# Kernel optimization log

Hardware: AMD Instinct MI355X
Metric: run time of the kernel (lower is better)

The kernel has to match this reference:

```python
import jax, jax.numpy as jnp
import numpy as np

CUTOFF = 6.0
NWAVE = 12
NTYPE = 2
DIMS = [36, 256, 128, 64, 32, 1]  # norbit -> hidden -> output


def setup_inputs() -> dict:
    key = jax.random.key(0)
    N, K = 8192, 48
    M = N * K
    ks = jax.random.split(key, 16)
    cart = jax.random.uniform(ks[0], (N, 3), jnp.float32, 0.0, 40.0)
    species = jax.random.randint(ks[1], (N,), 0, NTYPE).astype(jnp.int32)
    center = jnp.repeat(jnp.arange(N, dtype=jnp.int32), K)          # row 0: center atom i
    off = jax.random.randint(ks[2], (M,), 1, N).astype(jnp.int32)
    neigh = jnp.mod(center + off, N)                                 # row 1: neighbor j != i
    neigh_list = jnp.stack([center, neigh], axis=0)
    shifts = jax.random.normal(ks[3], (M, 3), jnp.float32)           # PBC shift vectors
    rs = jnp.tile(jnp.linspace(0.0, CUTOFF, NWAVE, dtype=jnp.float32), (NTYPE, 1))
    inta = -0.5 * jnp.ones((NTYPE, NWAVE), jnp.float32)              # gaussian exponents (negative)
    cparams = jnp.ones((NTYPE, NWAVE), jnp.float32)                  # embedded-atom coefficients
    params = {}
    kidx = 4
    for i in range(4):  # 4 hidden layers, stacked over [3 nets, ntype]
        fi, fo = DIMS[i], DIMS[i + 1]
        params[f'w{i+1}'] = jax.random.normal(ks[kidx], (3, NTYPE, fi, fo), jnp.float32) / np.sqrt(fi)
        params[f'b{i+1}'] = jnp.zeros((3, NTYPE, fo), jnp.float32)
        params[f'a{i+1}'] = jnp.ones((3, NTYPE, fo), jnp.float32)    # Relu_like alpha
        params[f'g{i+1}'] = jnp.ones((3, NTYPE, fo), jnp.float32)    # Relu_like beta
        kidx += 1
    params['wout'] = jax.random.normal(ks[kidx], (3, NTYPE, DIMS[4], 1), jnp.float32) / np.sqrt(DIMS[4])
    params['bout'] = jnp.zeros((3, NTYPE, 1), jnp.float32)
    return dict(cart=cart, shifts=shifts, rs=rs, inta=inta, cparams=cparams,
                **params, species=species, neigh_list=neigh_list)


def density_fn(cart, shifts, rs, inta, cparams, species, neigh_list):
    # EANN GetDensity: radial gaussians * cosine cutoff * angular monomials, scattered to centers.
    N = cart.shape[0]
    i, j = neigh_list[0], neigh_list[1]
    dvec = cart[i] - cart[j] + shifts                                 # [M,3]
    dist = jnp.linalg.norm(dvec, axis=-1)                             # [M]
    fc = jnp.square(0.5 * jnp.cos(dist * (jnp.pi / CUTOFF)) + 0.5)    # cutoff_cosine
    # angular basis: L=0 (1), L=1 (3), L=2 (9) -> 13 components, each premultiplied by fc
    ang = jnp.concatenate([
        fc[:, None],
        fc[:, None] * dvec,
        fc[:, None] * (dvec[:, :, None] * dvec[:, None, :]).reshape(-1, 9),
    ], axis=1)                                                        # [M,13]
    sj = species[j]
    gauss = jnp.exp(inta[sj] * jnp.square(dist[:, None] - rs[sj])) * cparams[sj]  # [M,NWAVE]
    worb = ang[:, :, None] * gauss[:, None, :]                        # [M,13,NWAVE]
    B = jax.ops.segment_sum(worb, i, num_segments=N)                  # [N,13,NWAVE]
    d0 = jnp.square(B[:, 0])                                          # L=0
    d1 = jnp.sum(jnp.square(B[:, 1:4]), axis=1)                       # L=1
    d2 = jnp.sum(jnp.square(B[:, 4:13]), axis=1)                      # L=2
    return jnp.concatenate([d0, d1, d2], axis=1)                      # [N,36]


def net_energy(density, species, layers, wout, bout):
    # per-atom-type MLP with Relu_like activation a*silu(g*x); run all types, select by species
    T = wout.shape[0]
    h = jnp.broadcast_to(density, (T,) + density.shape)               # [T,N,36]
    for (w, b, a, g) in layers:
        h = jnp.einsum('tnf,tfo->tno', h, w) + b[:, None, :]
        h = a[:, None, :] * jax.nn.silu(g[:, None, :] * h)
    out = jnp.einsum('tnf,tfo->tno', h, wout) + bout[:, None, :]      # [T,N,1]
    per_atom = jnp.take_along_axis(out[..., 0].T, species[:, None].astype(jnp.int32), axis=1)[:, 0]
    return jnp.sum(per_atom)


def reference(cart, shifts, rs, inta, cparams,
              w1, b1, a1, g1, w2, b2, a2, g2, w3, b3, a3, g3, w4, b4, a4, g4,
              wout, bout, species, neigh_list):
    def energy(c, n):
        d = density_fn(c, shifts, rs, inta, cparams, species, neigh_list)
        layers = [(w1[n], b1[n], a1[n], g1[n]), (w2[n], b2[n], a2[n], g2[n]),
                  (w3[n], b3[n], a3[n], g3[n]), (w4[n], b4[n], a4[n], g4[n])]
        return net_energy(d, species, layers, wout[n], bout[n])

    jab1 = jax.grad(lambda c: energy(c, 0))(cart)                     # dE0/dcart (create_graph analogue)
    jab2 = jax.grad(lambda c: energy(c, 1))(cart)                     # dE1/dcart
    e2 = energy(cart, 2)
    polar = jnp.einsum('ij,ik->jk', cart, jab1)
    polar = polar + polar.T + jnp.einsum('ij,ik->jk', jab2, jab2)
    polar = polar + e2 * jnp.eye(3, dtype=polar.dtype)
    return polar
```

## Files before the change

kernel.cpp:

```cpp
#include <hip/hip_runtime.h>

#define NWAVE 12
#define NL 13
#define NBW (NL*NWAVE)
#define D0 36
#define D1 256
#define D2 128
#define D3 64
#define D4 32
#define AT 16
#define NMAX 8192
#define NBSC 128
#define PI6 0.52359877559829887307f

#define F4(p) (*(const float4*)(p))
#define F2(p) (*(const float2*)(p))

__device__ __forceinline__ float wave_reduce(float v){
  #pragma unroll
  for(int o=32;o>0;o>>=1) v += __shfl_down(v,o);
  return v;
}

__global__ void perm_kernel(const int* __restrict__ species, int* __restrict__ perm,
                            int* __restrict__ counts, int N){
  __shared__ int sc[256];
  int t = threadIdx.x;
  int per = N/256;
  int c0 = 0;
  for(int k=0;k<per;k++) c0 += (species[t*per+k]==0) ? 1 : 0;
  sc[t]=c0; __syncthreads();
  for(int off=1; off<256; off<<=1){
    int add = (t>=off)? sc[t-off] : 0;
    __syncthreads();
    sc[t] += add;
    __syncthreads();
  }
  int incl = sc[t];
  int excl = incl - c0;
  int total0 = sc[255];
  if(t==0){ counts[0]=total0; counts[1]=N-total0; }
  int base0 = excl;
  int base1 = N + (t*per - excl);
  for(int k=0;k<per;k++){
    int a = t*per+k;
    if(species[a]==0) perm[base0++]=a; else perm[base1++]=a;
  }
}

__global__ void transpose_all_kernel(const float* __restrict__ w1, const float* __restrict__ w2,
                                     const float* __restrict__ w3, const float* __restrict__ w4,
                                     float* __restrict__ t1, float* __restrict__ t2,
                                     float* __restrict__ t3, float* __restrict__ t4){
  const int E1 = 6*D0*D1, E2 = 6*D1*D2, E3 = 6*D2*D3, E4 = 6*D3*D4;
  int idx = blockIdx.x*256 + threadIdx.x;
  if(idx < E1){
    int slab = idx/(D0*D1), r = idx%(D0*D1);
    int f = r/D1, o = r%D1;
    t1[slab*D0*D1 + o*D0 + f] = w1[idx];
  } else if(idx < E1+E2){
    int k = idx-E1; int slab = k/(D1*D2), r = k%(D1*D2);
    int f = r/D2, o = r%D2;
    t2[slab*D1*D2 + o*D1 + f] = w2[k];
  } else if(idx < E1+E2+E3){
    int k = idx-E1-E2; int slab = k/(D2*D3), r = k%(D2*D3);
    int f = r/D3, o = r%D3;
    t3[slab*D2*D3 + o*D2 + f] = w3[k];
  } else if(idx < E1+E2+E3+E4){
    int k = idx-E1-E2-E3; int slab = k/(D3*D4), r = k%(D3*D4);
    int f = r/D4, o = r%D4;
    t4[slab*D3*D4 + o*D3 + f] = w4[k];
  }
}

__global__ void pairs_kernel(const float* __restrict__ cart, const float* __restrict__ shifts,
                             const int* __restrict__ species, const int* __restrict__ neighJ,
                             float4* __restrict__ pairbuf, int M, int N, int K){
  extern __shared__ float4 ca[];
  int t = threadIdx.x;
  for(int a=t; a<N; a+=blockDim.x)
    ca[a] = make_float4(cart[a*3+0], cart[a*3+1], cart[a*3+2], (float)species[a]);
  __syncthreads();
  int stride = gridDim.x*blockDim.x;
  for(int m = blockIdx.x*blockDim.x + t; m < M; m += stride){
    int i = m / K;
    int j = neighJ[m];
    float4 cj = ca[j];
    float4 ci = ca[i];
    float dx = ci.x - cj.x + shifts[m*3+0];
    float dy = ci.y - cj.y + shifts[m*3+1];
    float dz = ci.z - cj.z + shifts[m*3+2];
    float dist = sqrtf(dx*dx+dy*dy+dz*dz);
    float enc = (cj.w != 0.f) ? -dist : dist;
    pairbuf[m] = make_float4(dx, dy, dz, enc);
  }
}

__launch_bounds__(256, 1)
__global__ void density_kernel(const float4* __restrict__ pairbuf,
                               const float* __restrict__ rs, const float* __restrict__ inta,
                               const float* __restrict__ cparams,
                               float* __restrict__ B, int K){
  int wv = threadIdx.x >> 6;
  int t  = threadIdx.x & 63;
  int i  = blockIdx.x*4 + wv;
  __shared__ float sang[4][64][NL];
  __shared__ float sg[4][64][NWAVE];
  if(t < K){
    float4 pb = pairbuf[(size_t)i*K + t];
    float dx = pb.x, dy = pb.y, dz = pb.z;
    int sj = (pb.w < 0.f) ? 1 : 0;
    float dist = fabsf(pb.w);
    float base = 0.5f*cosf(dist*PI6)+0.5f;
    float fc = base*base;
    #pragma unroll
    for(int w=0;w<NWAVE;w++){
      float d = dist - rs[sj*NWAVE+w];
      sg[wv][t][w] = __expf(inta[sj*NWAVE+w]*d*d)*cparams[sj*NWAVE+w];
    }
    sang[wv][t][0]=fc;
    sang[wv][t][1]=fc*dx;  sang[wv][t][2]=fc*dy;  sang[wv][t][3]=fc*dz;
    sang[wv][t][4]=fc*dx*dx; sang[wv][t][5]=fc*dx*dy; sang[wv][t][6]=fc*dx*dz;
    sang[wv][t][7]=fc*dy*dx; sang[wv][t][8]=fc*dy*dy; sang[wv][t][9]=fc*dy*dz;
    sang[wv][t][10]=fc*dz*dx; sang[wv][t][11]=fc*dz*dy; sang[wv][t][12]=fc*dz*dz;
  }
  __syncthreads();
  for(int idx=t; idx<NBW; idx+=64){
    int l = idx/NWAVE, w = idx%NWAVE;
    float s = 0.f;
    for(int k=0;k<K;k++) s += sang[wv][k][l]*sg[wv][k][w];
    B[(size_t)i*NBW+idx] = s;
  }
}

__launch_bounds__(256, 1)
__global__ void mlp_kernel(const float* __restrict__ B,
    const int* __restrict__ perm, const int* __restrict__ counts,
    const float* __restrict__ w1,const float* __restrict__ b1,const float* __restrict__ a1,const float* __restrict__ g1,
    const float* __restrict__ w2,const float* __restrict__ b2,const float* __restrict__ a2,const float* __restrict__ g2,
    const float* __restrict__ w3,const float* __restrict__ b3,const float* __restrict__ a3,const float* __restrict__ g3,
    const float* __restrict__ w4,const float* __restrict__ b4,const float* __restrict__ a4,const float* __restrict__ g4,
    const float* __restrict__ wout,const float* __restrict__ bout,
    const float* __restrict__ wt1,const float* __restrict__ wt2,const float* __restrict__ wt3,const float* __restrict__ wt4,
    float* __restrict__ G1, float* __restrict__ G2, float* __restrict__ e2acc, int N)
{
  const int bpt = N/AT;
  const int net = blockIdx.x / (2*bpt);
  const int rem = blockIdx.x % (2*bpt);
  const int typ = rem / bpt;
  const int sbase = (rem % bpt)*AT;
  const int cnt = counts[typ];
  if(sbase >= cnt) return;
  const int tid = threadIdx.x;
  const int slab = net*2 + typ;

  __shared__ __align__(16) float X[AT][D0];
  __shared__ __align__(16) float H1s[AT*D1];
  __shared__ __align__(16) float H2s[AT*D2];
  __shared__ __align__(16) float H3s[AT*D3];
  __shared__ __align__(16) float H4s[AT*D4];
  __shared__ int atomsS[AT];

  if(tid < AT){
    int slot = sbase + tid;
    atomsS[tid] = (slot < cnt) ? perm[typ*N + slot] : -1;
  }
  __syncthreads();

  for(int idx=tid; idx<AT*D0; idx+=256){
    int r = idx/D0, f = idx%D0;
    int a = atomsS[r];
    float v = 0.f;
    if(a >= 0){
      int w = f%NWAVE, grp = f/NWAVE;
      const float* Br = B + a*NBW;
      if(grp==0){ float b0=Br[w]; v=b0*b0; }
      else if(grp==1){
        #pragma unroll
        for(int l=1;l<4;l++){ float b0=Br[l*NWAVE+w]; v += b0*b0; }
      } else {
        #pragma unroll
        for(int l=4;l<13;l++){ float b0=Br[l*NWAVE+w]; v += b0*b0; }
      }
    }
    X[r][f] = v;
  }
  __syncthreads();

  const int l1c = (tid & 63)*4,  l1r = (tid >> 6)*4;
  const int l2c = (tid & 63)*2,  l2r = (tid >> 6)*4;
  const int l3c = (tid & 31)*2,  l3r = (tid >> 5)*2;
  const int l4c = (tid & 31),    l4r = (tid >> 5)*2;

  float A1r[4][4], A2r[4][2], A3r[2][2], A4r[2];

  {
    const float* W = w1 + slab*D0*D1;
    float acc[4][4];
    {
      float4 bv = F4(&b1[slab*D1+l1c]);
      #pragma unroll
      for(int rr=0;rr<4;rr++){ acc[rr][0]=bv.x; acc[rr][1]=bv.y; acc[rr][2]=bv.z; acc[rr][3]=bv.w; }
    }
    #pragma unroll
    for(int kk=0; kk<D0/4; kk++){
      float4 wa = F4(&W[(kk*4+0)*D1+l1c]);
      float4 wb = F4(&W[(kk*4+1)*D1+l1c]);
      float4 wc = F4(&W[(kk*4+2)*D1+l1c]);
      float4 wd = F4(&W[(kk*4+3)*D1+l1c]);
      #pragma unroll
      for(int rr=0;rr<4;rr++){
        float4 xv = F4(&X[l1r+rr][kk*4]);
        acc[rr][0] += xv.x*wa.x + xv.y*wb.x + xv.z*wc.x + xv.w*wd.x;
        acc[rr][1] += xv.x*wa.y + xv.y*wb.y + xv.z*wc.y + xv.w*wd.y;
        acc[rr][2] += xv.x*wa.z + xv.y*wb.z + xv.z*wc.z + xv.w*wd.z;
        acc[rr][3] += xv.x*wa.w + xv.y*wb.w + xv.z*wc.w + xv.w*wd.w;
      }
    }
    float4 av4 = F4(&a1[slab*D1+l1c]);
    float4 gv4 = F4(&g1[slab*D1+l1c]);
    float avv[4] = {av4.x, av4.y, av4.z, av4.w};
    float gvv[4] = {gv4.x, gv4.y, gv4.z, gv4.w};
    #pragma unroll
    for(int rr=0;rr<4;rr++){
      float hp[4];
      #pragma unroll
      for(int cc=0;cc<4;cc++){
        float u = gvv[cc]*acc[rr][cc];
        float s = 1.f/(1.f+__expf(-u));
        hp[cc] = avv[cc]*u*s;
        A1r[rr][cc] = avv[cc]*gvv[cc]*s*(1.f + u*(1.f-s));
      }
      float4 h; h.x=hp[0]; h.y=hp[1]; h.z=hp[2]; h.w=hp[3];
      *(float4*)&H1s[(l1r+rr)*D1 + l1c] = h;
    }
  }
  __syncthreads();
  {
    const float* W = w2 + slab*D1*D2;
    float acc[4][2];
    {
      float2 bv = F2(&b2[slab*D2+l2c]);
      #pragma unroll
      for(int rr=0;rr<4;rr++){ acc[rr][0]=bv.x; acc[rr][1]=bv.y; }
    }
    for(int kk=0; kk<D1/4; kk++){
      float2 wa = F2(&W[(kk*4+0)*D2+l2c]);
      float2 wb = F2(&W[(kk*4+1)*D2+l2c]);
      float2 wc = F2(&W[(kk*4+2)*D2+l2c]);
      float2 wd = F2(&W[(kk*4+3)*D2+l2c]);
      #pragma unroll
      for(int rr=0;rr<4;rr++){
        float4 hv = F4(&H1s[(l2r+rr)*D1 + kk*4]);
        acc[rr][0] += hv.x*wa.x + hv.y*wb.x + hv.z*wc.x + hv.w*wd.x;
        acc[rr][1] += hv.x*wa.y + hv.y*wb.y + hv.z*wc.y + hv.w*wd.y;
      }
    }
    float2 av2 = F2(&a2[slab*D2+l2c]);
    float2 gv2 = F2(&g2[slab*D2+l2c]);
    float avv[2] = {av2.x, av2.y};
    float gvv[2] = {gv2.x, gv2.y};
    #pragma unroll
    for(int rr=0;rr<4;rr++){
      float hp[2];
      #pragma unroll
      for(int cc=0;cc<2;cc++){
        float u = gvv[cc]*acc[rr][cc];
        float s = 1.f/(1.f+__expf(-u));
        hp[cc] = avv[cc]*u*s;
        A2r[rr][cc] = avv[cc]*gvv[cc]*s*(1.f + u*(1.f-s));
      }
      float2 h; h.x=hp[0]; h.y=hp[1];
      *(float2*)&H2s[(l2r+rr)*D2 + l2c] = h;
    }
  }
  __syncthreads();
  {
    const float* W = w3 + slab*D2*D3;
    float acc[2][2];
    {
      float2 bv = F2(&b3[slab*D3+l3c]);
      #pragma unroll
      for(int rr=0;rr<2;rr++){ acc[rr][0]=bv.x; acc[rr][1]=bv.y; }
    }
    for(int kk=0; kk<D2/4; kk++){
      float2 wa = F2(&W[(kk*4+0)*D3+l3c]);
      float2 wb = F2(&W[(kk*4+1)*D3+l3c]);
      float2 wc = F2(&W[(kk*4+2)*D3+l3c]);
      float2 wd = F2(&W[(kk*4+3)*D3+l3c]);
      #pragma unroll
      for(int rr=0;rr<2;rr++){
        float4 hv = F4(&H2s[(l3r+rr)*D2 + kk*4]);
        acc[rr][0] += hv.x*wa.x + hv.y*wb.x + hv.z*wc.x + hv.w*wd.x;
        acc[rr][1] += hv.x*wa.y + hv.y*wb.y + hv.z*wc.y + hv.w*wd.y;
      }
    }
    float2 av2 = F2(&a3[slab*D3+l3c]);
    float2 gv2 = F2(&g3[slab*D3+l3c]);
    float avv[2] = {av2.x, av2.y};
    float gvv[2] = {gv2.x, gv2.y};
    #pragma unroll
    for(int rr=0;rr<2;rr++){
      float hp[2];
      #pragma unroll
      for(int cc=0;cc<2;cc++){
        float u = gvv[cc]*acc[rr][cc];
        float s = 1.f/(1.f+__expf(-u));
        hp[cc] = avv[cc]*u*s;
        A3r[rr][cc] = avv[cc]*gvv[cc]*s*(1.f + u*(1.f-s));
      }
      float2 h; h.x=hp[0]; h.y=hp[1];
      *(float2*)&H3s[(l3r+rr)*D3 + l3c] = h;
    }
  }
  __syncthreads();
  {
    const float* W = w4 + slab*D3*D4;
    float bias = b4[slab*D4+l4c];
    float acc[2] = {bias, bias};
    for(int kk=0; kk<D3/4; kk++){
      float wa = W[(kk*4+0)*D4+l4c];
      float wb = W[(kk*4+1)*D4+l4c];
      float wc = W[(kk*4+2)*D4+l4c];
      float wd = W[(kk*4+3)*D4+l4c];
      #pragma unroll
      for(int rr=0;rr<2;rr++){
        float4 hv = F4(&H3s[(l4r+rr)*D3 + kk*4]);
        acc[rr] += hv.x*wa + hv.y*wb + hv.z*wc + hv.w*wd;
      }
    }
    float av = a4[slab*D4+l4c], gv = g4[slab*D4+l4c];
    #pragma unroll
    for(int rr=0;rr<2;rr++){
      float u = gv*acc[rr];
      float s = 1.f/(1.f+__expf(-u));
      H4s[(l4r+rr)*D4+l4c] = av*u*s;
      A4r[rr] = av*gv*s*(1.f + u*(1.f-s));
    }
  }
  __syncthreads();
  {
    const float* wo = wout + slab*D4;
    float val = 0.f;
    if(tid < AT){
      float s = bout[slab];
      const float* hr = &H4s[tid*D4];
      #pragma unroll
      for(int f=0;f<D4;f++) s += hr[f]*wo[f];
      if(net==2 && atomsS[tid]>=0) val = s;
    }
    if(net==2 && tid < 64){
      float v = wave_reduce(val);
      if(tid==0) atomicAdd(e2acc, v);
    }
  }
  if(net < 2){
    float* __restrict__ Gout = (net==0)? G1 : G2;
    const float* wo = wout + slab*D4;
    __syncthreads();
    {
      float wv = wo[l4c];
      H3s[(l4r+0)*D4+l4c] = wv * A4r[0];
      H3s[(l4r+1)*D4+l4c] = wv * A4r[1];
    }
    __syncthreads();
    {
      const float* WT = wt4 + slab*D4*D3;
      float acc[2][2] = {{0.f,0.f},{0.f,0.f}};
      #pragma unroll
      for(int kk=0; kk<D4/4; kk++){
        float2 wa = F2(&WT[(kk*4+0)*D3+l3c]);
        float2 wb = F2(&WT[(kk*4+1)*D3+l3c]);
        float2 wc = F2(&WT[(kk*4+2)*D3+l3c]);
        float2 wd = F2(&WT[(kk*4+3)*D3+l3c]);
        #pragma unroll
        for(int rr=0;rr<2;rr++){
          float4 dv = F4(&H3s[(l3r+rr)*D4 + kk*4]);
          acc[rr][0] += dv.x*wa.x + dv.y*wb.x + dv.z*wc.x + dv.w*wd.x;
          acc[rr][1] += dv.x*wa.y + dv.y*wb.y + dv.z*wc.y + dv.w*wd.y;
        }
      }
      #pragma unroll
      for(int rr=0;rr<2;rr++){
        float2 h;
        h.x = acc[rr][0]*A3r[rr][0];
        h.y = acc[rr][1]*A3r[rr][1];
        *(float2*)&H1s[(l3r+rr)*D3 + l3c] = h;
      }
    }
    __syncthreads();
    {
      const float* WT = wt3 + slab*D3*D2;
      float acc[4][2] = {{0.f,0.f},{0.f,0.f},{0.f,0.f},{0.f,0.f}};
      for(int kk=0; kk<D3/4; kk++){
        float2 wa = F2(&WT[(kk*4+0)*D2+l2c]);
        float2 wb = F2(&WT[(kk*4+1)*D2+l2c]);
        float2 wc = F2(&WT[(kk*4+2)*D2+l2c]);
        float2 wd = F2(&WT[(kk*4+3)*D2+l2c]);
        #pragma unroll
        for(int rr=0;rr<4;rr++){
          float4 dv = F4(&H1s[(l2r+rr)*D3 + kk*4]);
          acc[rr][0] += dv.x*wa.x + dv.y*wb.x + dv.z*wc.x + dv.w*wd.x;
          acc[rr][1] += dv.x*wa.y + dv.y*wb.y + dv.z*wc.y + dv.w*wd.y;
        }
      }
      #pragma unroll
      for(int rr=0;rr<4;rr++){
        float2 h;
        h.x = acc[rr][0]*A2r[rr][0];
        h.y = acc[rr][1]*A2r[rr][1];
        *(float2*)&H2s[(l2r+rr)*D2 + l2c] = h;
      }
    }
    __syncthreads();
    {
      const float* WT = wt2 + slab*D2*D1;
      float acc[4][4];
      #pragma unroll
      for(int rr=0;rr<4;rr++){ acc[rr][0]=0.f; acc[rr][1]=0.f; acc[rr][2]=0.f; acc[rr][3]=0.f; }
      for(int kk=0; kk<D2/4; kk++){
        float4 wa = F4(&WT[(kk*4+0)*D1+l1c]);
        float4 wb = F4(&WT[(kk*4+1)*D1+l1c]);
        float4 wc = F4(&WT[(kk*4+2)*D1+l1c]);
        float4 wd = F4(&WT[(kk*4+3)*D1+l1c]);
        #pragma unroll
        for(int rr=0;rr<4;rr++){
          float4 dv = F4(&H2s[(l1r+rr)*D2 + kk*4]);
          acc[rr][0] += dv.x*wa.x + dv.y*wb.x + dv.z*wc.x + dv.w*wd.x;
          acc[rr][1] += dv.x*wa.y + dv.y*wb.y + dv.z*wc.y + dv.w*wd.y;
          acc[rr][2] += dv.x*wa.z + dv.y*wb.z + dv.z*wc.z + dv.w*wd.z;
          acc[rr][3] += dv.x*wa.w + dv.y*wb.w + dv.z*wc.w + dv.w*wd.w;
        }
      }
      #pragma unroll
      for(int rr=0;rr<4;rr++){
        float4 h;
        h.x = acc[rr][0]*A1r[rr][0];
        h.y = acc[rr][1]*A1r[rr][1];
        h.z = acc[rr][2]*A1r[rr][2];
        h.w = acc[rr][3]*A1r[rr][3];
        *(float4*)&H1s[(l1r+rr)*D1 + l1c] = h;
      }
    }
    __syncthreads();
    {
      const float* WT = wt1 + slab*D1*D0;
      for(int idx=tid; idx<AT*D0; idx+=256){
        int r = idx/D0, f = idx%D0;
        const float* dr = &H1s[r*D1];
        float acc = 0.f;
        for(int oo=0; oo<D1; oo+=4){
          const float4 dv = F4(&dr[oo]);
          acc += dv.x*WT[(oo+0)*D0+f] + dv.y*WT[(oo+1)*D0+f]
               + dv.z*WT[(oo+2)*D0+f] + dv.w*WT[(oo+3)*D0+f];
        }
        int a = atomsS[r];
        if(a >= 0) Gout[a*D0+f] = acc;
      }
    }
  }
}

__launch_bounds__(256, 1)
__global__ void pair_back_kernel(const float4* __restrict__ pairbuf,
                                 const float* __restrict__ shifts,
                                 const float* __restrict__ rs, const float* __restrict__ inta,
                                 const float* __restrict__ cparams,
                                 const float* __restrict__ B,
                                 const float* __restrict__ G1, const float* __restrict__ G2,
                                 float* __restrict__ Ppart, float* __restrict__ jab2c,
                                 float* __restrict__ f2buf, int K){
  int wv = threadIdx.x >> 6;
  int t  = threadIdx.x & 63;
  int i  = blockIdx.x*4 + wv;
  __shared__ float E1[4][NBW], E2[4][NBW];
  for(int idx=t; idx<NBW; idx+=64){
    int l = idx/NWAVE, w = idx%NWAVE;
    int grp = (l==0) ? 0 : ((l<4) ? 1 : 2);
    float b = B[(size_t)i*NBW+idx];
    E1[wv][idx] = 2.f*b*G1[(size_t)i*D0 + grp*NWAVE + w];
    E2[wv][idx] = 2.f*b*G2[(size_t)i*D0 + grp*NWAVE + w];
  }
  __syncthreads();
  float p[9] = {0.f,0.f,0.f,0.f,0.f,0.f,0.f,0.f,0.f};
  float fi2[3] = {0.f,0.f,0.f};
  if(t < K){
    int m = i*K + t;
    float4 pb = pairbuf[(size_t)m];
    float dx = pb.x, dy = pb.y, dz = pb.z;
    int sj = (pb.w < 0.f) ? 1 : 0;
    float dist = fabsf(pb.w);
    float shx = shifts[m*3+0], shy = shifts[m*3+1], shz = shifts[m*3+2];
    float invd = 1.f/dist;
    float u = dist*PI6;
    float base = 0.5f*cosf(u)+0.5f;
    float fc = base*base;
    float fcp = -PI6*sinf(u)*base;
    float gs[NWAVE], tw[NWAVE];
    #pragma unroll
    for(int w=0;w<NWAVE;w++){
      float d = dist - rs[sj*NWAVE+w];
      float ia = inta[sj*NWAVE+w];
      float g = __expf(ia*d*d)*cparams[sj*NWAVE+w];
      gs[w] = g;
      tw[w] = fcp*g + fc*(2.f*ia*d*g);
    }
    float mono[NL] = {1.f, dx,dy,dz, dx*dx,dx*dy,dx*dz, dy*dx,dy*dy,dy*dz, dz*dx,dz*dy,dz*dz};
    float f1[3], f2[3];
    for(int net=0; net<2; net++){
      const float* E = net ? E2[wv] : E1[wv];
      float sl[NL];
      float radial = 0.f;
      #pragma unroll
      for(int l=0;l<NL;l++){
        float s = 0.f, q = 0.f;
        #pragma unroll
        for(int w=0;w<NWAVE;w++){
          float e = E[l*NWAVE+w];
          s += e*gs[w];
          q += e*tw[w];
        }
        sl[l] = s;
        radial += mono[l]*q;
      }
      float Ax = sl[1] + 2.f*sl[4]*dx + (sl[5]+sl[7])*dy + (sl[6]+sl[10])*dz;
      float Ay = sl[2] + (sl[5]+sl[7])*dx + 2.f*sl[8]*dy + (sl[9]+sl[11])*dz;
      float Az = sl[3] + (sl[6]+sl[10])*dx + (sl[9]+sl[11])*dy + 2.f*sl[12]*dz;
      float rr = radial*invd;
      float fx = dx*rr + fc*Ax;
      float fy = dy*rr + fc*Ay;
      float fz = dz*rr + fc*Az;
      if(net==0){ f1[0]=fx; f1[1]=fy; f1[2]=fz; }
      else      { f2[0]=fx; f2[1]=fy; f2[2]=fz; }
    }
    float cx = dx-shx, cy = dy-shy, cz = dz-shz;
    p[0]=cx*f1[0]; p[1]=cx*f1[1]; p[2]=cx*f1[2];
    p[3]=cy*f1[0]; p[4]=cy*f1[1]; p[5]=cy*f1[2];
    p[6]=cz*f1[0]; p[7]=cz*f1[1]; p[8]=cz*f1[2];
    float* fb = f2buf + (size_t)m*3;
    fb[0]=f2[0]; fb[1]=f2[1]; fb[2]=f2[2];
    fi2[0]=f2[0]; fi2[1]=f2[1]; fi2[2]=f2[2];
  }
  #pragma unroll
  for(int k=0;k<9;k++){
    float v = wave_reduce(p[k]);
    if(t==0) Ppart[(size_t)i*9+k] = v;
  }
  #pragma unroll
  for(int c=0;c<3;c++){
    float v = wave_reduce(fi2[c]);
    if(t==0) jab2c[(size_t)i*3+c] = v;
  }
}

__global__ void scatter_kernel(const int* __restrict__ neighJ, const float* __restrict__ f2buf,
                               float* __restrict__ jpart, int M, int N){
  __shared__ float lds[NMAX];
  int b = blockIdx.x, t = threadIdx.x;
  int chunk = (M + gridDim.x - 1) / gridDim.x;
  int m0 = b*chunk;
  int m1 = m0 + chunk; if(m1 > M) m1 = M;
  for(int c=0;c<3;c++){
    for(int n=t; n<N; n+=256) lds[n] = 0.f;
    __syncthreads();
    for(int m=m0+t; m<m1; m+=256)
      atomicAdd(&lds[neighJ[m]], -f2buf[(size_t)m*3+c]);
    __syncthreads();
    float* dst = jpart + ((size_t)b*3 + c)*N;
    for(int n=t; n<N; n+=256) dst[n] = lds[n];
    __syncthreads();
  }
}

__global__ void reduce_kernel(const float* __restrict__ Ppart, const float* __restrict__ jab2c,
                              const float* __restrict__ jpart,
                              float* __restrict__ Pacc, float* __restrict__ S2, int N){
  __shared__ float red[256];
  int tid = threadIdx.x;
  float s2[9] = {0.f,0.f,0.f,0.f,0.f,0.f,0.f,0.f,0.f};
  float pp[9] = {0.f,0.f,0.f,0.f,0.f,0.f,0.f,0.f,0.f};
  for(int n = blockIdx.x*256 + tid; n < N; n += gridDim.x*256){
    float x = jab2c[n*3+0], y = jab2c[n*3+1], z = jab2c[n*3+2];
    for(int b=0;b<NBSC;b++){
      const float* jp = jpart + (size_t)b*3*N;
      x += jp[0*(size_t)N + n];
      y += jp[1*(size_t)N + n];
      z += jp[2*(size_t)N + n];
    }
    s2[0]+=x*x; s2[1]+=x*y; s2[2]+=x*z;
    s2[3]+=y*x; s2[4]+=y*y; s2[5]+=y*z;
    s2[6]+=z*x; s2[7]+=z*y; s2[8]+=z*z;
    const float* pr = Ppart + (size_t)n*9;
    #pragma unroll
    for(int k=0;k<9;k++) pp[k] += pr[k];
  }
  #pragma unroll
  for(int k=0;k<9;k++){
    red[tid]=s2[k]; __syncthreads();
    for(int off=128; off>0; off>>=1){
      if(tid<off) red[tid]+=red[tid+off];
      __syncthreads();
    }
    if(tid==0) atomicAdd(&S2[k], red[0]);
    __syncthreads();
    red[tid]=pp[k]; __syncthreads();
    for(int off=128; off>0; off>>=1){
      if(tid<off) red[tid]+=red[tid+off];
      __syncthreads();
    }
    if(tid==0) atomicAdd(&Pacc[k], red[0]);
    __syncthreads();
  }
}

__global__ void final_kernel(const float* __restrict__ Pacc, const float* __restrict__ S2,
                             const float* __restrict__ e2acc, float* __restrict__ out){
  int tid = threadIdx.x;
  if(tid < 9){
    int a = tid/3, b = tid%3;
    float v = Pacc[a*3+b] + Pacc[b*3+a] + S2[tid];
    if(a==b) v += e2acc[0];
    out[tid] = v;
  }
}

extern "C" void kernel_launch(void* const* d_in, const int* in_sizes, int n_in,
                              void* d_out, int out_size, void* d_ws, size_t ws_size,
                              hipStream_t stream){
  const float* cart    = (const float*)d_in[0];
  const float* shifts  = (const float*)d_in[1];
  const float* rs      = (const float*)d_in[2];
  const float* inta    = (const float*)d_in[3];
  const float* cparams = (const float*)d_in[4];
  const float* w1 = (const float*)d_in[5];
  const float* b1 = (const float*)d_in[6];
  const float* a1 = (const float*)d_in[7];
  const float* g1 = (const float*)d_in[8];
  const float* w2 = (const float*)d_in[9];
  const float* b2 = (const float*)d_in[10];
  const float* a2 = (const float*)d_in[11];
  const float* g2 = (const float*)d_in[12];
  const float* w3 = (const float*)d_in[13];
  const float* b3 = (const float*)d_in[14];
  const float* a3 = (const float*)d_in[15];
  const float* g3 = (const float*)d_in[16];
  const float* w4 = (const float*)d_in[17];
  const float* b4 = (const float*)d_in[18];
  const float* a4 = (const float*)d_in[19];
  const float* g4 = (const float*)d_in[20];
  const float* wout = (const float*)d_in[21];
  const float* bout = (const float*)d_in[22];
  const int* species = (const int*)d_in[23];
  const int* neigh   = (const int*)d_in[24];
  float* out = (float*)d_out;

  const int N = in_sizes[0]/3;
  const int M = in_sizes[24]/2;
  const int K = M/N;
  const int* neighJ = neigh + M;

  char* base = (char*)d_ws;
  size_t off = 0;
  auto alloc = [&](size_t bytes)->void*{
    void* p = base + off;
    off = (off + bytes + 255) & ~(size_t)255;
    return p;
  };
  float*  Bws    = (float*)alloc((size_t)N*NBW*4);
  float*  G1ws   = (float*)alloc((size_t)N*D0*4);
  float*  G2ws   = (float*)alloc((size_t)N*D0*4);
  float*  Ppart  = (float*)alloc((size_t)N*9*4);
  float*  jab2c  = (float*)alloc((size_t)N*3*4);
  float*  f2buf  = (float*)alloc((size_t)M*3*4);
  float4* pairbuf= (float4*)alloc((size_t)M*16);
  float*  jpart  = (float*)alloc((size_t)NBSC*3*N*4);
  float*  acc    = (float*)alloc(32*4);
  int*    counts = (int*)alloc(2*4);
  int*    perm   = (int*)alloc((size_t)2*N*4);
  float*  WT1    = (float*)alloc((size_t)6*D0*D1*4);
  float*  WT2    = (float*)alloc((size_t)6*D1*D2*4);
  float*  WT3    = (float*)alloc((size_t)6*D2*D3*4);
  float*  WT4    = (float*)alloc((size_t)6*D3*D4*4);

  hipMemsetAsync(acc, 0, 32*4, stream);

  size_t ldsBytes = (size_t)N*16;
  hipFuncSetAttribute((const void*)pairs_kernel,
                      hipFuncAttributeMaxDynamicSharedMemorySize, (int)ldsBytes);

  const int ETOT = 6*(D0*D1 + D1*D2 + D2*D3 + D3*D4);
  perm_kernel<<<1,256,0,stream>>>(species, perm, counts, N);
  transpose_all_kernel<<<(ETOT+255)/256,256,0,stream>>>(w1,w2,w3,w4, WT1,WT2,WT3,WT4);
  pairs_kernel<<<256,1024,ldsBytes,stream>>>(cart, shifts, species, neighJ, pairbuf, M, N, K);
  density_kernel<<<N/4,256,0,stream>>>(pairbuf, rs, inta, cparams, Bws, K);
  mlp_kernel<<<3*2*(N/AT),256,0,stream>>>(Bws, perm, counts,
      w1,b1,a1,g1, w2,b2,a2,g2, w3,b3,a3,g3, w4,b4,a4,g4, wout,bout,
      WT1,WT2,WT3,WT4, G1ws,G2ws, acc+18, N);
  pair_back_kernel<<<N/4,256,0,stream>>>(pairbuf, shifts, rs, inta, cparams,
                                         Bws, G1ws, G2ws, Ppart, jab2c, f2buf, K);
  scatter_kernel<<<NBSC,256,0,stream>>>(neighJ, f2buf, jpart, M, N);
  reduce_kernel<<<64,256,0,stream>>>(Ppart, jab2c, jpart, acc, acc+9, N);
  final_kernel<<<1,64,0,stream>>>(acc, acc+9, acc+18, out);
}
```

Measured before the change: 284.9 us.

## Make MLP kernel wave-private per atom rows, replacing block barriers with wave syncs

Each wavefront of the MLP kernel now owns four atom rows across every forward and backward layer, so all shared-memory traffic stays within that wave. Block-wide __syncthreads are replaced by an lgkmcnt wait plus a scheduling barrier. Layers 3 and 4 and their backward passes are remapped so each lane handles one column for four rows, and the energy reduction is done per wave. This removes cross-wave barrier stalls, at the cost of a different thread-to-work mapping and narrower weight loads in layer 3, and it relies on the lgkmcnt wait being enough to order LDS accesses within a wave.

```diff
diff --git a/kernel.cpp b/kernel.cpp
--- a/kernel.cpp
+++ b/kernel.cpp
@@ -15,6 +15,9 @@
 
 #define F4(p) (*(const float4*)(p))
 #define F2(p) (*(const float2*)(p))
+
+#define WSYNC() do{ asm volatile("s_waitcnt lgkmcnt(0)" ::: "memory"); \
+                    __builtin_amdgcn_sched_barrier(0); }while(0)
 
 __device__ __forceinline__ float wave_reduce(float v){
   #pragma unroll
@@ -152,6 +155,9 @@
   const int cnt = counts[typ];
   if(sbase >= cnt) return;
   const int tid = threadIdx.x;
+  const int wv  = tid >> 6;
+  const int ln  = tid & 63;
+  const int r0  = wv*4;
   const int slab = net*2 + typ;
 
   __shared__ __align__(16) float X[AT][D0];
@@ -161,15 +167,15 @@
   __shared__ __align__(16) float H4s[AT*D4];
   __shared__ int atomsS[AT];
 
-  if(tid < AT){
-    int slot = sbase + tid;
-    atomsS[tid] = (slot < cnt) ? perm[typ*N + slot] : -1;
-  }
-  __syncthreads();
-
-  for(int idx=tid; idx<AT*D0; idx+=256){
+  if(ln < 4){
+    int slot = sbase + r0 + ln;
+    atomsS[r0+ln] = (slot < cnt) ? perm[typ*N + slot] : -1;
+  }
+  WSYNC();
+
+  for(int idx=ln; idx<4*D0; idx+=64){
     int r = idx/D0, f = idx%D0;
-    int a = atomsS[r];
+    int a = atomsS[r0+r];
     float v = 0.f;
     if(a >= 0){
       int w = f%NWAVE, grp = f/NWAVE;
@@ -183,16 +189,17 @@
         for(int l=4;l<13;l++){ float b0=Br[l*NWAVE+w]; v += b0*b0; }
       }
     }
-    X[r][f] = v;
-  }
-  __syncthreads();
-
-  const int l1c = (tid & 63)*4,  l1r = (tid >> 6)*4;
-  const int l2c = (tid & 63)*2,  l2r = (tid >> 6)*4;
-  const int l3c = (tid & 31)*2,  l3r = (tid >> 5)*2;
-  const int l4c = (tid & 31),    l4r = (tid >> 5)*2;
-
-  float A1r[4][4], A2r[4][2], A3r[2][2], A4r[2];
+    X[r0+r][f] = v;
+  }
+  WSYNC();
+
+  const int l1c = ln*4;
+  const int l2c = ln*2;
+  const int l3c = ln;
+  const int l4c = ln & 31;
+  const int l4r = (ln >> 5)*2;
+
+  float A1r[4][4], A2r[4][2], A3r[4], A4r[2];
 
   {
     const float* W = w1 + slab*D0*D1;
@@ -210,7 +217,7 @@
       float4 wd = F4(&W[(kk*4+3)*D1+l1c]);
       #pragma unroll
       for(int rr=0;rr<4;rr++){
-        float4 xv = F4(&X[l1r+rr][kk*4]);
+        float4 xv = F4(&X[r0+rr][kk*4]);
         acc[rr][0] += xv.x*wa.x + xv.y*wb.x + xv.z*wc.x + xv.w*wd.x;
         acc[rr][1] += xv.x*wa.y + xv.y*wb.y + xv.z*wc.y + xv.w*wd.y;
         acc[rr][2] += xv.x*wa.z + xv.y*wb.z + xv.z*wc.z + xv.w*wd.z;
@@ -232,10 +239,10 @@
         A1r[rr][cc] = avv[cc]*gvv[cc]*s*(1.f + u*(1.f-s));
       }
       float4 h; h.x=hp[0]; h.y=hp[1]; h.z=hp[2]; h.w=hp[3];
-      *(float4*)&H1s[(l1r+rr)*D1 + l1c] = h;
-    }
-  }
-  __syncthreads();
+      *(float4*)&H1s[(r0+rr)*D1 + l1c] = h;
+    }
+  }
+  WSYNC();
   {
     const float* W = w2 + slab*D1*D2;
     float acc[4][2];
@@ -251,7 +258,7 @@
       float2 wd = F2(&W[(kk*4+3)*D2+l2c]);
       #pragma unroll
       for(int rr=0;rr<4;rr++){
-        float4 hv = F4(&H1s[(l2r+rr)*D1 + kk*4]);
+        float4 hv = F4(&H1s[(r0+rr)*D1 + kk*4]);
         acc[rr][0] += hv.x*wa.x + hv.y*wb.x + hv.z*wc.x + hv.w*wd.x;
         acc[rr][1] += hv.x*wa.y + hv.y*wb.y + hv.z*wc.y + hv.w*wd.y;
       }
@@ -271,49 +278,35 @@
         A2r[rr][cc] = avv[cc]*gvv[cc]*s*(1.f + u*(1.f-s));
       }
       float2 h; h.x=hp[0]; h.y=hp[1];
-      *(float2*)&H2s[(l2r+rr)*D2 + l2c] = h;
-    }
-  }
-  __syncthreads();
+      *(float2*)&H2s[(r0+rr)*D2 + l2c] = h;
+    }
+  }
+  WSYNC();
   {
     const float* W = w3 + slab*D2*D3;
-    float acc[2][2];
-    {
-      float2 bv = F2(&b3[slab*D3+l3c]);
-      #pragma unroll
-      for(int rr=0;rr<2;rr++){ acc[rr][0]=bv.x; acc[rr][1]=bv.y; }
-    }
+    float bias = b3[slab*D3+l3c];
+    float acc[4] = {bias, bias, bias, bias};
     for(int kk=0; kk<D2/4; kk++){
-      float2 wa = F2(&W[(kk*4+0)*D3+l3c]);
-      float2 wb = F2(&W[(kk*4+1)*D3+l3c]);
-      float2 wc = F2(&W[(kk*4+2)*D3+l3c]);
-      float2 wd = F2(&W[(kk*4+3)*D3+l3c]);
-      #pragma unroll
-      for(int rr=0;rr<2;rr++){
-        float4 hv = F4(&H2s[(l3r+rr)*D2 + kk*4]);
-        acc[rr][0] += hv.x*wa.x + hv.y*wb.x + hv.z*wc.x + hv.w*wd.x;
-        acc[rr][1] += hv.x*wa.y + hv.y*wb.y + hv.z*wc.y + hv.w*wd.y;
-      }
-    }
-    float2 av2 = F2(&a3[slab*D3+l3c]);
-    float2 gv2 = F2(&g3[slab*D3+l3c]);
-    float avv[2] = {av2.x, av2.y};
-    float gvv[2] = {gv2.x, gv2.y};
-    #pragma unroll
-    for(int rr=0;rr<2;rr++){
-      float hp[2];
-      #pragma unroll
-      for(int cc=0;cc<2;cc++){
-        float u = gvv[cc]*acc[rr][cc];
-        float s = 1.f/(1.f+__expf(-u));
-        hp[cc] = avv[cc]*u*s;
-        A3r[rr][cc] = avv[cc]*gvv[cc]*s*(1.f + u*(1.f-s));
-      }
-      float2 h; h.x=hp[0]; h.y=hp[1];
-      *(float2*)&H3s[(l3r+rr)*D3 + l3c] = h;
-    }
-  }
-  __syncthreads();
+      float wa = W[(kk*4+0)*D3+l3c];
+      float wb = W[(kk*4+1)*D3+l3c];
+      float wc = W[(kk*4+2)*D3+l3c];
+      float wd = W[(kk*4+3)*D3+l3c];
+      #pragma unroll
+      for(int rr=0;rr<4;rr++){
+        float4 hv = F4(&H2s[(r0+rr)*D2 + kk*4]);
+        acc[rr] += hv.x*wa + hv.y*wb + hv.z*wc + hv.w*wd;
+      }
+    }
+    float av = a3[slab*D3+l3c], gv = g3[slab*D3+l3c];
+    #pragma unroll
+    for(int rr=0;rr<4;rr++){
+      float u = gv*acc[rr];
+      float s = 1.f/(1.f+__expf(-u));
+      H3s[(r0+rr)*D3+l3c] = av*u*s;
+      A3r[rr] = av*gv*s*(1.f + u*(1.f-s));
+    }
+  }
+  WSYNC();
   {
     const float* W = w4 + slab*D3*D4;
     float bias = b4[slab*D4+l4c];
@@ -325,7 +318,7 @@
       float wd = W[(kk*4+3)*D4+l4c];
       #pragma unroll
       for(int rr=0;rr<2;rr++){
-        float4 hv = F4(&H3s[(l4r+rr)*D3 + kk*4]);
+        float4 hv = F4(&H3s[(r0+l4r+rr)*D3 + kk*4]);
         acc[rr] += hv.x*wa + hv.y*wb + hv.z*wc + hv.w*wd;
       }
     }
@@ -334,61 +327,56 @@
     for(int rr=0;rr<2;rr++){
       float u = gv*acc[rr];
       float s = 1.f/(1.f+__expf(-u));
-      H4s[(l4r+rr)*D4+l4c] = av*u*s;
+      H4s[(r0+l4r+rr)*D4+l4c] = av*u*s;
       A4r[rr] = av*gv*s*(1.f + u*(1.f-s));
     }
   }
-  __syncthreads();
-  {
+  WSYNC();
+  if(net == 2){
     const float* wo = wout + slab*D4;
     float val = 0.f;
-    if(tid < AT){
-      float s = bout[slab];
-      const float* hr = &H4s[tid*D4];
-      #pragma unroll
-      for(int f=0;f<D4;f++) s += hr[f]*wo[f];
-      if(net==2 && atomsS[tid]>=0) val = s;
-    }
-    if(net==2 && tid < 64){
-      float v = wave_reduce(val);
-      if(tid==0) atomicAdd(e2acc, v);
-    }
+    if(ln < 4){
+      int a = atomsS[r0+ln];
+      if(a >= 0){
+        float s = bout[slab];
+        const float* hr = &H4s[(r0+ln)*D4];
+        #pragma unroll
+        for(int f=0;f<D4;f++) s += hr[f]*wo[f];
+        val = s;
+      }
+    }
+    float v = wave_reduce(val);
+    if(ln==0) atomicAdd(e2acc, v);
   }
   if(net < 2){
     float* __restrict__ Gout = (net==0)? G1 : G2;
     const float* wo = wout + slab*D4;
-    __syncthreads();
     {
-      float wv = wo[l4c];
-      H3s[(l4r+0)*D4+l4c] = wv * A4r[0];
-      H3s[(l4r+1)*D4+l4c] = wv * A4r[1];
-    }
-    __syncthreads();
+      float wv4 = wo[l4c];
+      H3s[(r0+l4r+0)*D3+l4c] = wv4 * A4r[0];
+      H3s[(r0+l4r+1)*D3+l4c] = wv4 * A4r[1];
+    }
+    WSYNC();
     {
       const float* WT = wt4 + slab*D4*D3;
-      float acc[2][2] = {{0.f,0.f},{0.f,0.f}};
+      float acc[4] = {0.f,0.f,0.f,0.f};
       #pragma unroll
       for(int kk=0; kk<D4/4; kk++){
-        float2 wa = F2(&WT[(kk*4+0)*D3+l3c]);
-        float2 wb = F2(&WT[(kk*4+1)*D3+l3c]);
-        float2 wc = F2(&WT[(kk*4+2)*D3+l3c]);
-        float2 wd = F2(&WT[(kk*4+3)*D3+l3c]);
+        float wa = WT[(kk*4+0)*D3+l3c];
+        float wb = WT[(kk*4+1)*D3+l3c];
+        float wc = WT[(kk*4+2)*D3+l3c];
+        float wd = WT[(kk*4+3)*D3+l3c];
         #pragma unroll
-        for(int rr=0;rr<2;rr++){
-          float4 dv = F4(&H3s[(l3r+rr)*D4 + kk*4]);
-          acc[rr][0] += dv.x*wa.x + dv.y*wb.x + dv.z*wc.x + dv.w*wd.x;
-          acc[rr][1] += dv.x*wa.y + dv.y*wb.y + dv.z*wc.y + dv.w*wd.y;
+        for(int rr=0;rr<4;rr++){
+          float4 dv = F4(&H3s[(r0+rr)*D3 + kk*4]);
+          acc[rr] += dv.x*wa + dv.y*wb + dv.z*wc + dv.w*wd;
         }
       }
       #pragma unroll
-      for(int rr=0;rr<2;rr++){
-        float2 h;
-        h.x = acc[rr][0]*A3r[rr][0];
-        h.y = acc[rr][1]*A3r[rr][1];
-        *(float2*)&H1s[(l3r+rr)*D3 + l3c] = h;
-      }
-    }
-    __syncthreads();
+      for(int rr=0;rr<4;rr++)
+        H1s[(r0+rr)*D1+l3c] = acc[rr]*A3r[rr];
+    }
+    WSYNC();
     {
       const float* WT = wt3 + slab*D3*D2;
       float acc[4][2] = {{0.f,0.f},{0.f,0.f},{0.f,0.f},{0.f,0.f}};
@@ -399,7 +387,7 @@
         float2 wd = F2(&WT[(kk*4+3)*D2+l2c]);
         #pragma unroll
         for(int rr=0;rr<4;rr++){
-          float4 dv = F4(&H1s[(l2r+rr)*D3 + kk*4]);
+          float4 dv = F4(&H1s[(r0+rr)*D1 + kk*4]);
           acc[rr][0] += dv.x*wa.x + dv.y*wb.x + dv.z*wc.x + dv.w*wd.x;
           acc[rr][1] += dv.x*wa.y + dv.y*wb.y + dv.z*wc.y + dv.w*wd.y;
         }
@@ -409,10 +397,10 @@
         float2 h;
         h.x = acc[rr][0]*A2r[rr][0];
         h.y = acc[rr][1]*A2r[rr][1];
-        *(float2*)&H2s[(l2r+rr)*D2 + l2c] = h;
-      }
-    }
-    __syncthreads();
+        *(float2*)&H2s[(r0+rr)*D2 + l2c] = h;
+      }
+    }
+    WSYNC();
     {
       const float* WT = wt2 + slab*D2*D1;
       float acc[4][4];
@@ -425,7 +413,7 @@
         float4 wd = F4(&WT[(kk*4+3)*D1+l1c]);
         #pragma unroll
         for(int rr=0;rr<4;rr++){
-          float4 dv = F4(&H2s[(l1r+rr)*D2 + kk*4]);
+          float4 dv = F4(&H2s[(r0+rr)*D2 + kk*4]);
           acc[rr][0] += dv.x*wa.x + dv.y*wb.x + dv.z*wc.x + dv.w*wd.x;
           acc[rr][1] += dv.x*wa.y + dv.y*wb.y + dv.z*wc.y + dv.w*wd.y;
           acc[rr][2] += dv.x*wa.z + dv.y*wb.z + dv.z*wc.z + dv.w*wd.z;
@@ -439,22 +427,22 @@
         h.y = acc[rr][1]*A1r[rr][1];
         h.z = acc[rr][2]*A1r[rr][2];
         h.w = acc[rr][3]*A1r[rr][3];
-        *(float4*)&H1s[(l1r+rr)*D1 + l1c] = h;
-      }
-    }
-    __syncthreads();
+        *(float4*)&H1s[(r0+rr)*D1 + l1c] = h;
+      }
+    }
+    WSYNC();
     {
       const float* WT = wt1 + slab*D1*D0;
-      for(int idx=tid; idx<AT*D0; idx+=256){
+      for(int idx=ln; idx<4*D0; idx+=64){
         int r = idx/D0, f = idx%D0;
-        const float* dr = &H1s[r*D1];
+        const float* dr = &H1s[(r0+r)*D1];
         float acc = 0.f;
         for(int oo=0; oo<D1; oo+=4){
           const float4 dv = F4(&dr[oo]);
           acc += dv.x*WT[(oo+0)*D0+f] + dv.y*WT[(oo+1)*D0+f]
                + dv.z*WT[(oo+2)*D0+f] + dv.w*WT[(oo+3)*D0+f];
         }
-        int a = atomsS[r];
+        int a = atomsS[r0+r];
         if(a >= 0) Gout[a*D0+f] = acc;
       }
     }
```

Result: no change. 280.3 us (-1.6%).
